# Kernel optimization log

Hardware: AMD Instinct MI355X
Metric: run time of the kernel (lower is better)

Reference implementation:

```python
import jax, jax.numpy as jnp
import numpy as np

N = 100000   # nodes
E = 1600000  # edges (avg degree 16)
D = 128      # input feature dim
H = 128      # Config.hidden_dim
G = 64       # graphs in batch
OUT = 2      # output classes


def setup_inputs() -> dict:
    key = jax.random.key(0)
    ks = jax.random.split(key, 12)
    s = 0.05
    return {
        "x": jax.random.normal(ks[0], (N, D), dtype=jnp.float32),
        "edge_index": jax.random.randint(ks[1], (2, E), 0, N),
        "batch": jnp.sort(jax.random.randint(ks[2], (N,), 0, G)),
        "W1": jax.random.normal(ks[3], (H, D), dtype=jnp.float32) * s,
        "b1": jnp.zeros((H,), jnp.float32),
        "W2": jax.random.normal(ks[4], (H, H), dtype=jnp.float32) * s,
        "b2": jnp.zeros((H,), jnp.float32),
        "Wf1": jax.random.normal(ks[5], (H, H), dtype=jnp.float32) * s,
        "bf1": jnp.zeros((H,), jnp.float32),
        "Wf2": jax.random.normal(ks[6], (OUT, H), dtype=jnp.float32) * s,
        "bf2": jnp.zeros((OUT,), jnp.float32),
    }


def _gnn_layer(x, src, dst, W, b):
    # message(x_j) = Linear(x[src]); linear commutes with gather, so transform
    # node features once (N rows) instead of per-edge (E rows): same math.
    xw = x @ W.T + b                                   # [N, H]
    msg = xw[src]                                      # [E, H] gather
    summed = jax.ops.segment_sum(msg, dst, num_segments=N)            # [N, H]
    cnt = jax.ops.segment_sum(jnp.ones((src.shape[0],), x.dtype), dst,
                              num_segments=N)                          # [N]
    return summed / jnp.maximum(cnt, 1.0)[:, None]     # scatter-mean (0 for deg-0)


def reference(x, edge_index, batch, W1, b1, W2, b2, Wf1, bf1, Wf2, bf2):
    src, dst = edge_index[0], edge_index[1]
    h = jax.nn.relu(_gnn_layer(x, src, dst, W1, b1))
    h = jax.nn.relu(_gnn_layer(h, src, dst, W2, b2))
    g = jax.ops.segment_max(h, batch, num_segments=G)  # global_max_pool [G, H]
    z = jax.nn.relu(g @ Wf1.T + bf1)                   # fc (dropout = identity, eval)
    z = z @ Wf2.T + bf2                                # [G, OUT]
    return jax.nn.log_softmax(z, axis=1)
```

## Files before the change

kernel.cpp:

```cpp
#include <hip/hip_runtime.h>
#include <hip/hip_fp16.h>
#include <math.h>


#define BUCKET_SHIFT 8
#define BUCKET_SIZE 256
#define MAXBUCK 512
#define BIN_CHUNK 4096
#define CAP 4608
#define LSTR 136

typedef _Float16 half8 __attribute__((ext_vector_type(8)));
typedef _Float16 half4v __attribute__((ext_vector_type(4)));
typedef _Float16 half2v __attribute__((ext_vector_type(2)));
typedef float floatx4 __attribute__((ext_vector_type(4)));
typedef float floatx2 __attribute__((ext_vector_type(2)));

#define RFL(v) __builtin_amdgcn_readfirstlane(v)

__global__ __launch_bounds__(256) void k_bin(
        const int* __restrict__ src, const int* __restrict__ dst,
        int* __restrict__ bcur, int* __restrict__ staging,
        const int* __restrict__ batch, int* __restrict__ gstart,
        int* __restrict__ gend,
        const float* __restrict__ W1, const float* __restrict__ W2,
        _Float16* __restrict__ w1h, _Float16* __restrict__ w2h,
        int E, int N, int nbuck) {
    __shared__ int lh[MAXBUCK];
    __shared__ int lbase[MAXBUCK];
    __shared__ int lc[MAXBUCK];
    int t = threadIdx.x;
    for (int i = t; i < nbuck; i += 256) { lh[i] = 0; lc[i] = 0; }

    if (blockIdx.x < 64) {
        int i = blockIdx.x * 256 + t;
        w1h[i] = (_Float16)W1[i];
        w2h[i] = (_Float16)W2[i];
    }

    int n = blockIdx.x * 256 + t;
    if (n < N) {
        int b = batch[n];
        if (n == 0 || batch[n - 1] != b) gstart[b] = n;
        if (n == N - 1 || batch[n + 1] != b) gend[b] = n + 1;
    }
    __syncthreads();

    int base = blockIdx.x * BIN_CHUNK;
    if (base + BIN_CHUNK <= E) {
        int ds[16], ss[16];
        const int4* dv = (const int4*)(dst + base);
        const int4* sv = (const int4*)(src + base);
        #pragma unroll
        for (int j = 0; j < 4; ++j) {
            int4 d = dv[j * 256 + t];
            int4 s = sv[j * 256 + t];
            ds[j * 4 + 0] = d.x; ds[j * 4 + 1] = d.y;
            ds[j * 4 + 2] = d.z; ds[j * 4 + 3] = d.w;
            ss[j * 4 + 0] = s.x; ss[j * 4 + 1] = s.y;
            ss[j * 4 + 2] = s.z; ss[j * 4 + 3] = s.w;
        }
        #pragma unroll
        for (int q = 0; q < 16; ++q)
            atomicAdd(&lh[ds[q] >> BUCKET_SHIFT], 1);
        __syncthreads();
        for (int i = t; i < nbuck; i += 256)
            if (lh[i]) lbase[i] = i * CAP + atomicAdd(&bcur[i], lh[i]);
        __syncthreads();
        #pragma unroll
        for (int q = 0; q < 16; ++q) {
            int d = ds[q];
            int b = d >> BUCKET_SHIFT;
            int pos = lbase[b] + atomicAdd(&lc[b], 1);
            if (pos < (b + 1) * CAP)
                staging[pos] = ss[q] | ((d & (BUCKET_SIZE - 1)) << 24);
        }
    } else {
        for (int e = base + t; e < E; e += 256)
            atomicAdd(&lh[dst[e] >> BUCKET_SHIFT], 1);
        __syncthreads();
        for (int i = t; i < nbuck; i += 256)
            if (lh[i]) lbase[i] = i * CAP + atomicAdd(&bcur[i], lh[i]);
        __syncthreads();
        for (int e = base + t; e < E; e += 256) {
            int d = dst[e];
            int b = d >> BUCKET_SHIFT;
            int pos = lbase[b] + atomicAdd(&lc[b], 1);
            if (pos < (b + 1) * CAP)
                staging[pos] = src[e] | ((d & (BUCKET_SIZE - 1)) << 24);
        }
    }
}

__global__ __launch_bounds__(BUCKET_SIZE) void k_bcsr(
        const int* __restrict__ staging, const int* __restrict__ bcur,
        int* __restrict__ esrc, int* __restrict__ rowstart,
        int* __restrict__ deg, int N) {
    __shared__ int sw[CAP];
    __shared__ int lh[BUCKET_SIZE];
    __shared__ int lcur[BUCKET_SIZE];
    __shared__ int wsum[4];
    int b = blockIdx.x;
    int s = b * CAP;
    int e = s + min(bcur[b], CAP);
    int len = e - s;
    int t = threadIdx.x;
    lh[t] = 0;
    __syncthreads();
    for (int i = t; i < len; i += BUCKET_SIZE) {
        int p = staging[s + i];
        sw[i] = p;
        atomicAdd(&lh[((unsigned)p) >> 24], 1);
    }
    __syncthreads();
    int v = lh[t];
    int lane = t & 63;
    int wv = t >> 6;
    int inc = v;
    #pragma unroll
    for (int off = 1; off < 64; off <<= 1) {
        int x = __shfl_up(inc, off, 64);
        if (lane >= off) inc += x;
    }
    if (lane == 63) wsum[wv] = inc;
    __syncthreads();
    int woff = 0;
    #pragma unroll
    for (int k = 0; k < 3; ++k)
        if (k < wv) woff += wsum[k];
    int excl = woff + inc - v;
    int node = b * BUCKET_SIZE + t;
    if (node < N) { rowstart[node] = s + excl; deg[node] = v; }
    lcur[t] = excl;
    __syncthreads();
    for (int i = t; i < len; i += BUCKET_SIZE) {
        int p = sw[i];
        int local = ((unsigned)p) >> 24;
        int pos = atomicAdd(&lcur[local], 1);
        esrc[s + pos] = p & 0xFFFFFF;
    }
}

template <typename T>
__global__ __launch_bounds__(512) void k_gemm(const T* __restrict__ in,
                                              const _Float16* __restrict__ Wh,
                                              const float* __restrict__ bias,
                                              unsigned char* __restrict__ out8,
                                              int N) {
    __shared__ _Float16 sX[128 * LSTR];
    __shared__ _Float16 sW[128 * LSTR];
    int t = threadIdx.x;

    #pragma unroll
    for (int it = 0; it < 8; ++it) {
        int lin = it * 512 + t;
        int r = lin >> 5;
        int c = (lin & 31) * 4;
        *(half4v*)&sW[r * LSTR + c] = *(const half4v*)(Wh + r * 128 + c);
    }

    int w = t >> 6;
    int lane = t & 63;
    int quad = lane >> 4;
    int lrow = lane & 15;

    #pragma unroll
    for (int tile = 0; tile < 2; ++tile) {
        int n0 = blockIdx.x * 256 + tile * 128;
        __syncthreads();
        #pragma unroll
        for (int it = 0; it < 8; ++it) {
            int lin = it * 512 + t;
            int r = lin >> 5;
            int c = (lin & 31) * 4;
            half4v xh = {0, 0, 0, 0};
            int n = n0 + r;
            if (n < N) {
                if constexpr (sizeof(T) == 4) {
                    float4 xv = *(const float4*)((const float*)in + (size_t)n * 128 + c);
                    xh = half4v{ (_Float16)xv.x, (_Float16)xv.y, (_Float16)xv.z, (_Float16)xv.w };
                } else {
                    xh = *(const half4v*)((const _Float16*)in + (size_t)n * 128 + c);
                }
            }
            *(half4v*)&sX[r * LSTR + c] = xh;
        }
        __syncthreads();

        floatx4 acc[8];
        #pragma unroll
        for (int i = 0; i < 8; ++i) acc[i] = {0.f, 0.f, 0.f, 0.f};

        int arow = (w * 16 + lrow) * LSTR + quad * 8;
        #pragma unroll
        for (int k0 = 0; k0 < 128; k0 += 32) {
            half8 a = *(const half8*)&sX[arow + k0];
            #pragma unroll
            for (int ht = 0; ht < 8; ++ht) {
                half8 bfr = *(const half8*)&sW[(ht * 16 + lrow) * LSTR + quad * 8 + k0];
                acc[ht] = __builtin_amdgcn_mfma_f32_16x16x32_f16(a, bfr, acc[ht], 0, 0, 0);
            }
        }

        #pragma unroll
        for (int ht = 0; ht < 8; ++ht) {
            int h = ht * 16 + lrow;
            float bv = bias[h];
            #pragma unroll
            for (int r = 0; r < 4; ++r) {
                int node = n0 + w * 16 + quad * 4 + r;
                if (node < N) {
                    float v = acc[ht][r] + bv;
                    int pk = __builtin_amdgcn_cvt_pk_fp8_f32(v, v, 0, false);
                    out8[(size_t)node * 128 + h] = (unsigned char)(pk & 0xFF);
                }
            }
        }
    }
}

__global__ __launch_bounds__(256) void k_agg(const unsigned char* __restrict__ in8,
                                             const int* __restrict__ esrc,
                                             const int* __restrict__ rowstart,
                                             const int* __restrict__ deg,
                                             _Float16* __restrict__ outh, int N) {
    int lane = threadIdx.x & 63;
    int node = blockIdx.x * 4 + (threadIdx.x >> 6);
    if (node >= N) return;
    int start = RFL(rowstart[node]);
    int d     = RFL(deg[node]);
    const unsigned short* in16 = (const unsigned short*)in8;

    floatx2 a0 = {0.f, 0.f}, a1 = {0.f, 0.f}, a2 = {0.f, 0.f}, a3 = {0.f, 0.f};

    int i = 0;
    for (; i + 8 <= d; i += 8) {
        int x0 = RFL(esrc[start + i + 0]);
        int x1 = RFL(esrc[start + i + 1]);
        int x2 = RFL(esrc[start + i + 2]);
        int x3 = RFL(esrc[start + i + 3]);
        int x4 = RFL(esrc[start + i + 4]);
        int x5 = RFL(esrc[start + i + 5]);
        int x6 = RFL(esrc[start + i + 6]);
        int x7 = RFL(esrc[start + i + 7]);
        unsigned u0 = in16[((size_t)x0 << 6) + lane];
        unsigned u1 = in16[((size_t)x1 << 6) + lane];
        unsigned u2 = in16[((size_t)x2 << 6) + lane];
        unsigned u3 = in16[((size_t)x3 << 6) + lane];
        unsigned u4 = in16[((size_t)x4 << 6) + lane];
        unsigned u5 = in16[((size_t)x5 << 6) + lane];
        unsigned u6 = in16[((size_t)x6 << 6) + lane];
        unsigned u7 = in16[((size_t)x7 << 6) + lane];
        floatx2 f0 = __builtin_amdgcn_cvt_pk_f32_fp8(u0, false);
        floatx2 f1 = __builtin_amdgcn_cvt_pk_f32_fp8(u1, false);
        floatx2 f2 = __builtin_amdgcn_cvt_pk_f32_fp8(u2, false);
        floatx2 f3 = __builtin_amdgcn_cvt_pk_f32_fp8(u3, false);
        floatx2 f4 = __builtin_amdgcn_cvt_pk_f32_fp8(u4, false);
        floatx2 f5 = __builtin_amdgcn_cvt_pk_f32_fp8(u5, false);
        floatx2 f6 = __builtin_amdgcn_cvt_pk_f32_fp8(u6, false);
        floatx2 f7 = __builtin_amdgcn_cvt_pk_f32_fp8(u7, false);
        a0.x += f0.x; a0.y += f0.y;  a1.x += f1.x; a1.y += f1.y;
        a2.x += f2.x; a2.y += f2.y;  a3.x += f3.x; a3.y += f3.y;
        a0.x += f4.x; a0.y += f4.y;  a1.x += f5.x; a1.y += f5.y;
        a2.x += f6.x; a2.y += f6.y;  a3.x += f7.x; a3.y += f7.y;
    }
    for (; i + 4 <= d; i += 4) {
        int x0 = RFL(esrc[start + i + 0]);
        int x1 = RFL(esrc[start + i + 1]);
        int x2 = RFL(esrc[start + i + 2]);
        int x3 = RFL(esrc[start + i + 3]);
        unsigned u0 = in16[((size_t)x0 << 6) + lane];
        unsigned u1 = in16[((size_t)x1 << 6) + lane];
        unsigned u2 = in16[((size_t)x2 << 6) + lane];
        unsigned u3 = in16[((size_t)x3 << 6) + lane];
        floatx2 f0 = __builtin_amdgcn_cvt_pk_f32_fp8(u0, false);
        floatx2 f1 = __builtin_amdgcn_cvt_pk_f32_fp8(u1, false);
        floatx2 f2 = __builtin_amdgcn_cvt_pk_f32_fp8(u2, false);
        floatx2 f3 = __builtin_amdgcn_cvt_pk_f32_fp8(u3, false);
        a0.x += f0.x; a0.y += f0.y;  a1.x += f1.x; a1.y += f1.y;
        a2.x += f2.x; a2.y += f2.y;  a3.x += f3.x; a3.y += f3.y;
    }
    for (; i < d; ++i) {
        int x0 = RFL(esrc[start + i]);
        unsigned u0 = in16[((size_t)x0 << 6) + lane];
        floatx2 f0 = __builtin_amdgcn_cvt_pk_f32_fp8(u0, false);
        a0.x += f0.x; a0.y += f0.y;
    }

    float sx = (a0.x + a1.x) + (a2.x + a3.x);
    float sy = (a0.y + a1.y) + (a2.y + a3.y);
    float dm = fmaxf((float)d, 1.0f);
    half2v r = { (_Float16)fmaxf(sx / dm, 0.f),
                 (_Float16)fmaxf(sy / dm, 0.f) };
    *(half2v*)(outh + (size_t)node * 128 + lane * 2) = r;
}

__global__ __launch_bounds__(256) void k_aggp2(const unsigned char* __restrict__ in8,
                                               const int* __restrict__ esrc,
                                               const int* __restrict__ rowstart,
                                               const int* __restrict__ deg,
                                               const int* __restrict__ batch,
                                               float* __restrict__ pm, int N) {
    int lane = threadIdx.x & 63;
    int gw = blockIdx.x * 4 + (threadIdx.x >> 6);
    int n0 = gw * 16;
    if (n0 >= N) return;
    int nend = min(n0 + 16, N);
    const unsigned short* in16 = (const unsigned short*)in8;

    int curg = RFL(batch[n0]);
    float mx = 0.f, my = 0.f;

    for (int node = n0; node < nend; ++node) {
        int g = RFL(batch[node]);
        if (g != curg) {
            int* pmi = (int*)(pm + (size_t)curg * 128 + lane * 2);
            atomicMax(pmi,     __float_as_int(mx));
            atomicMax(pmi + 1, __float_as_int(my));
            curg = g; mx = 0.f; my = 0.f;
        }
        int start = RFL(rowstart[node]);
        int d     = RFL(deg[node]);
        floatx2 a0 = {0.f, 0.f}, a1 = {0.f, 0.f}, a2 = {0.f, 0.f}, a3 = {0.f, 0.f};
        int i = 0;
        for (; i + 8 <= d; i += 8) {
            int x0 = RFL(esrc[start + i + 0]);
            int x1 = RFL(esrc[start + i + 1]);
            int x2 = RFL(esrc[start + i + 2]);
            int x3 = RFL(esrc[start + i + 3]);
            int x4 = RFL(esrc[start + i + 4]);
            int x5 = RFL(esrc[start + i + 5]);
            int x6 = RFL(esrc[start + i + 6]);
            int x7 = RFL(esrc[start + i + 7]);
            unsigned u0 = in16[((size_t)x0 << 6) + lane];
            unsigned u1 = in16[((size_t)x1 << 6) + lane];
            unsigned u2 = in16[((size_t)x2 << 6) + lane];
            unsigned u3 = in16[((size_t)x3 << 6) + lane];
            unsigned u4 = in16[((size_t)x4 << 6) + lane];
            unsigned u5 = in16[((size_t)x5 << 6) + lane];
            unsigned u6 = in16[((size_t)x6 << 6) + lane];
            unsigned u7 = in16[((size_t)x7 << 6) + lane];
            floatx2 f0 = __builtin_amdgcn_cvt_pk_f32_fp8(u0, false);
            floatx2 f1 = __builtin_amdgcn_cvt_pk_f32_fp8(u1, false);
            floatx2 f2 = __builtin_amdgcn_cvt_pk_f32_fp8(u2, false);
            floatx2 f3 = __builtin_amdgcn_cvt_pk_f32_fp8(u3, false);
            floatx2 f4 = __builtin_amdgcn_cvt_pk_f32_fp8(u4, false);
            floatx2 f5 = __builtin_amdgcn_cvt_pk_f32_fp8(u5, false);
            floatx2 f6 = __builtin_amdgcn_cvt_pk_f32_fp8(u6, false);
            floatx2 f7 = __builtin_amdgcn_cvt_pk_f32_fp8(u7, false);
            a0.x += f0.x; a0.y += f0.y;  a1.x += f1.x; a1.y += f1.y;
            a2.x += f2.x; a2.y += f2.y;  a3.x += f3.x; a3.y += f3.y;
            a0.x += f4.x; a0.y += f4.y;  a1.x += f5.x; a1.y += f5.y;
            a2.x += f6.x; a2.y += f6.y;  a3.x += f7.x; a3.y += f7.y;
        }
        for (; i + 4 <= d; i += 4) {
            int x0 = RFL(esrc[start + i + 0]);
            int x1 = RFL(esrc[start + i + 1]);
            int x2 = RFL(esrc[start + i + 2]);
            int x3 = RFL(esrc[start + i + 3]);
            unsigned u0 = in16[((size_t)x0 << 6) + lane];
            unsigned u1 = in16[((size_t)x1 << 6) + lane];
            unsigned u2 = in16[((size_t)x2 << 6) + lane];
            unsigned u3 = in16[((size_t)x3 << 6) + lane];
            floatx2 f0 = __builtin_amdgcn_cvt_pk_f32_fp8(u0, false);
            floatx2 f1 = __builtin_amdgcn_cvt_pk_f32_fp8(u1, false);
            floatx2 f2 = __builtin_amdgcn_cvt_pk_f32_fp8(u2, false);
            floatx2 f3 = __builtin_amdgcn_cvt_pk_f32_fp8(u3, false);
            a0.x += f0.x; a0.y += f0.y;  a1.x += f1.x; a1.y += f1.y;
            a2.x += f2.x; a2.y += f2.y;  a3.x += f3.x; a3.y += f3.y;
        }
        for (; i < d; ++i) {
            int x0 = RFL(esrc[start + i]);
            unsigned u0 = in16[((size_t)x0 << 6) + lane];
            floatx2 f0 = __builtin_amdgcn_cvt_pk_f32_fp8(u0, false);
            a0.x += f0.x; a0.y += f0.y;
        }
        float sx = (a0.x + a1.x) + (a2.x + a3.x);
        float sy = (a0.y + a1.y) + (a2.y + a3.y);
        float dm = fmaxf((float)d, 1.0f);
        mx = fmaxf(mx, fmaxf(sx / dm, 0.f));
        my = fmaxf(my, fmaxf(sy / dm, 0.f));
    }
    int* pmi = (int*)(pm + (size_t)curg * 128 + lane * 2);
    atomicMax(pmi,     __float_as_int(mx));
    atomicMax(pmi + 1, __float_as_int(my));
}

__global__ void k_fc(const float* __restrict__ pm,
                     const float* __restrict__ Wf1, const float* __restrict__ bf1,
                     const float* __restrict__ Wf2, const float* __restrict__ bf2,
                     float* __restrict__ out) {
    __shared__ float sg[128];
    __shared__ float sz[128];
    __shared__ float so[2];
    int g = blockIdx.x;
    int t = threadIdx.x;
    sg[t] = pm[(size_t)g * 128 + t];
    __syncthreads();
    float z = bf1[t];
    #pragma unroll 4
    for (int d = 0; d < 128; ++d)
        z += sg[d] * Wf1[t * 128 + d];
    sz[t] = fmaxf(z, 0.f);
    __syncthreads();
    if (t < 2) {
        float o = bf2[t];
        for (int d = 0; d < 128; ++d)
            o += sz[d] * Wf2[t * 128 + d];
        so[t] = o;
    }
    __syncthreads();
    if (t == 0) {
        float a = so[0], b = so[1];
        float mx = fmaxf(a, b);
        float ls = mx + logf(expf(a - mx) + expf(b - mx));
        out[g * 2 + 0] = a - ls;
        out[g * 2 + 1] = b - ls;
    }
}

extern "C" void kernel_launch(void* const* d_in, const int* in_sizes, int n_in,
                              void* d_out, int out_size, void* d_ws, size_t ws_size,
                              hipStream_t stream) {
    const float* x   = (const float*)d_in[0];
    const int*   ei  = (const int*)d_in[1];
    const int* batch = (const int*)d_in[2];
    const float* W1  = (const float*)d_in[3];
    const float* b1  = (const float*)d_in[4];
    const float* W2  = (const float*)d_in[5];
    const float* b2  = (const float*)d_in[6];
    const float* Wf1 = (const float*)d_in[7];
    const float* bf1 = (const float*)d_in[8];
    const float* Wf2 = (const float*)d_in[9];
    const float* bf2 = (const float*)d_in[10];

    int N = in_sizes[2];
    int E = in_sizes[1] / 2;
    int G = out_size / 2;
    const int* src = ei;
    const int* dst = ei + E;
    int nbuck = (N + BUCKET_SIZE - 1) / BUCKET_SIZE;

    char* p = (char*)d_ws;
    auto alloc = [&](size_t bytes) -> char* {
        char* r = p;
        p += (bytes + 255) & ~(size_t)255;
        return r;
    };
    unsigned char* A  = (unsigned char*)alloc((size_t)N * 128);
    unsigned char* A2 = (unsigned char*)alloc((size_t)N * 128);
    _Float16* B    = (_Float16*)alloc((size_t)N * 128 * 2);
    int* deg       = (int*)alloc((size_t)N * 4);
    int* rowstart  = (int*)alloc((size_t)N * 4);
    int* esrc      = (int*)alloc((size_t)nbuck * CAP * 4);
    int* staging   = (int*)alloc((size_t)nbuck * CAP * 4);
    _Float16* w1h  = (_Float16*)alloc((size_t)128 * 128 * 2);
    _Float16* w2h  = (_Float16*)alloc((size_t)128 * 128 * 2);
    char* zbase    = p;
    int* bcur      = (int*)alloc((size_t)MAXBUCK * 4);
    int* gstart    = (int*)alloc((size_t)G * 4);
    int* gend      = (int*)alloc((size_t)G * 4);
    float* pm      = (float*)alloc((size_t)G * 128 * 4);
    size_t zbytes  = (size_t)(p - zbase);

    int nchunk = (E + BIN_CHUNK - 1) / BIN_CHUNK;

    hipMemsetAsync(zbase, 0, zbytes, stream);
    k_bin<<<nchunk, 256, 0, stream>>>(src, dst, bcur, staging, batch,
                                      gstart, gend, W1, W2, w1h, w2h,
                                      E, N, nbuck);
    k_bcsr<<<nbuck, BUCKET_SIZE, 0, stream>>>(staging, bcur, esrc, rowstart, deg, N);

    k_gemm<float><<<(N + 255) / 256, 512, 0, stream>>>(x, w1h, b1, A, N);
    k_agg<<<(N + 3) / 4, 256, 0, stream>>>(A, esrc, rowstart, deg, B, N);
    k_gemm<_Float16><<<(N + 255) / 256, 512, 0, stream>>>(B, w2h, b2, A2, N);
    k_aggp2<<<(N + 63) / 64, 256, 0, stream>>>(A2, esrc, rowstart, deg, batch, pm, N);
    k_fc<<<G, 128, 0, stream>>>(pm, Wf1, bf1, Wf2, bf2, (float*)d_out);
}
```

Before: 284.0 us.

## Fuse layer-1 aggregation with layer-2 GEMM to skip fp16 intermediate

Merges the first scatter-mean aggregation kernel and the second-layer GEMM into one kernel. Each wave aggregates 16 nodes into shared memory, then runs MFMA against W2 read directly from global memory and writes fp8 output. This removes the N×128 fp16 intermediate buffer write and read and one kernel launch. In exchange each wave now processes 16 nodes serially before its GEMM step, so there are fewer waves in flight to hide gather latency, and W2 is no longer staged in LDS.

```diff
diff --git a/kernel.cpp b/kernel.cpp
--- a/kernel.cpp
+++ b/kernel.cpp
@@ -141,8 +141,7 @@
     }
 }
 
-template <typename T>
-__global__ __launch_bounds__(512) void k_gemm(const T* __restrict__ in,
+__global__ __launch_bounds__(512) void k_gemm(const float* __restrict__ in,
                                               const _Float16* __restrict__ Wh,
                                               const float* __restrict__ bias,
                                               unsigned char* __restrict__ out8,
@@ -176,12 +175,8 @@
             half4v xh = {0, 0, 0, 0};
             int n = n0 + r;
             if (n < N) {
-                if constexpr (sizeof(T) == 4) {
-                    float4 xv = *(const float4*)((const float*)in + (size_t)n * 128 + c);
-                    xh = half4v{ (_Float16)xv.x, (_Float16)xv.y, (_Float16)xv.z, (_Float16)xv.w };
-                } else {
-                    xh = *(const half4v*)((const _Float16*)in + (size_t)n * 128 + c);
-                }
+                float4 xv = *(const float4*)(in + (size_t)n * 128 + c);
+                xh = half4v{ (_Float16)xv.x, (_Float16)xv.y, (_Float16)xv.z, (_Float16)xv.w };
             }
             *(half4v*)&sX[r * LSTR + c] = xh;
         }
@@ -219,80 +214,123 @@
     }
 }
 
-__global__ __launch_bounds__(256) void k_agg(const unsigned char* __restrict__ in8,
+__global__ __launch_bounds__(256) void k_agf(const unsigned char* __restrict__ in8,
                                              const int* __restrict__ esrc,
                                              const int* __restrict__ rowstart,
                                              const int* __restrict__ deg,
-                                             _Float16* __restrict__ outh, int N) {
-    int lane = threadIdx.x & 63;
-    int node = blockIdx.x * 4 + (threadIdx.x >> 6);
-    if (node >= N) return;
-    int start = RFL(rowstart[node]);
-    int d     = RFL(deg[node]);
+                                             const _Float16* __restrict__ w2h,
+                                             const float* __restrict__ b2,
+                                             unsigned char* __restrict__ out8,
+                                             int N) {
+    __shared__ _Float16 sX[64 * LSTR];
+    int t = threadIdx.x;
+    int w = t >> 6;
+    int lane = t & 63;
+    int n0 = blockIdx.x * 64 + w * 16;
     const unsigned short* in16 = (const unsigned short*)in8;
 
-    floatx2 a0 = {0.f, 0.f}, a1 = {0.f, 0.f}, a2 = {0.f, 0.f}, a3 = {0.f, 0.f};
-
-    int i = 0;
-    for (; i + 8 <= d; i += 8) {
-        int x0 = RFL(esrc[start + i + 0]);
-        int x1 = RFL(esrc[start + i + 1]);
-        int x2 = RFL(esrc[start + i + 2]);
-        int x3 = RFL(esrc[start + i + 3]);
-        int x4 = RFL(esrc[start + i + 4]);
-        int x5 = RFL(esrc[start + i + 5]);
-        int x6 = RFL(esrc[start + i + 6]);
-        int x7 = RFL(esrc[start + i + 7]);
-        unsigned u0 = in16[((size_t)x0 << 6) + lane];
-        unsigned u1 = in16[((size_t)x1 << 6) + lane];
-        unsigned u2 = in16[((size_t)x2 << 6) + lane];
-        unsigned u3 = in16[((size_t)x3 << 6) + lane];
-        unsigned u4 = in16[((size_t)x4 << 6) + lane];
-        unsigned u5 = in16[((size_t)x5 << 6) + lane];
-        unsigned u6 = in16[((size_t)x6 << 6) + lane];
-        unsigned u7 = in16[((size_t)x7 << 6) + lane];
-        floatx2 f0 = __builtin_amdgcn_cvt_pk_f32_fp8(u0, false);
-        floatx2 f1 = __builtin_amdgcn_cvt_pk_f32_fp8(u1, false);
-        floatx2 f2 = __builtin_amdgcn_cvt_pk_f32_fp8(u2, false);
-        floatx2 f3 = __builtin_amdgcn_cvt_pk_f32_fp8(u3, false);
-        floatx2 f4 = __builtin_amdgcn_cvt_pk_f32_fp8(u4, false);
-        floatx2 f5 = __builtin_amdgcn_cvt_pk_f32_fp8(u5, false);
-        floatx2 f6 = __builtin_amdgcn_cvt_pk_f32_fp8(u6, false);
-        floatx2 f7 = __builtin_amdgcn_cvt_pk_f32_fp8(u7, false);
-        a0.x += f0.x; a0.y += f0.y;  a1.x += f1.x; a1.y += f1.y;
-        a2.x += f2.x; a2.y += f2.y;  a3.x += f3.x; a3.y += f3.y;
-        a0.x += f4.x; a0.y += f4.y;  a1.x += f5.x; a1.y += f5.y;
-        a2.x += f6.x; a2.y += f6.y;  a3.x += f7.x; a3.y += f7.y;
-    }
-    for (; i + 4 <= d; i += 4) {
-        int x0 = RFL(esrc[start + i + 0]);
-        int x1 = RFL(esrc[start + i + 1]);
-        int x2 = RFL(esrc[start + i + 2]);
-        int x3 = RFL(esrc[start + i + 3]);
-        unsigned u0 = in16[((size_t)x0 << 6) + lane];
-        unsigned u1 = in16[((size_t)x1 << 6) + lane];
-        unsigned u2 = in16[((size_t)x2 << 6) + lane];
-        unsigned u3 = in16[((size_t)x3 << 6) + lane];
-        floatx2 f0 = __builtin_amdgcn_cvt_pk_f32_fp8(u0, false);
-        floatx2 f1 = __builtin_amdgcn_cvt_pk_f32_fp8(u1, false);
-        floatx2 f2 = __builtin_amdgcn_cvt_pk_f32_fp8(u2, false);
-        floatx2 f3 = __builtin_amdgcn_cvt_pk_f32_fp8(u3, false);
-        a0.x += f0.x; a0.y += f0.y;  a1.x += f1.x; a1.y += f1.y;
-        a2.x += f2.x; a2.y += f2.y;  a3.x += f3.x; a3.y += f3.y;
-    }
-    for (; i < d; ++i) {
-        int x0 = RFL(esrc[start + i]);
-        unsigned u0 = in16[((size_t)x0 << 6) + lane];
-        floatx2 f0 = __builtin_amdgcn_cvt_pk_f32_fp8(u0, false);
-        a0.x += f0.x; a0.y += f0.y;
-    }
-
-    float sx = (a0.x + a1.x) + (a2.x + a3.x);
-    float sy = (a0.y + a1.y) + (a2.y + a3.y);
-    float dm = fmaxf((float)d, 1.0f);
-    half2v r = { (_Float16)fmaxf(sx / dm, 0.f),
-                 (_Float16)fmaxf(sy / dm, 0.f) };
-    *(half2v*)(outh + (size_t)node * 128 + lane * 2) = r;
+    for (int k = 0; k < 16; ++k) {
+        int node = n0 + k;
+        float sx = 0.f, sy = 0.f;
+        int dd = 0;
+        if (node < N) {
+            int start = RFL(rowstart[node]);
+            int d     = RFL(deg[node]);
+            dd = d;
+            floatx2 a0 = {0.f, 0.f}, a1 = {0.f, 0.f}, a2 = {0.f, 0.f}, a3 = {0.f, 0.f};
+            int i = 0;
+            for (; i + 8 <= d; i += 8) {
+                int x0 = RFL(esrc[start + i + 0]);
+                int x1 = RFL(esrc[start + i + 1]);
+                int x2 = RFL(esrc[start + i + 2]);
+                int x3 = RFL(esrc[start + i + 3]);
+                int x4 = RFL(esrc[start + i + 4]);
+                int x5 = RFL(esrc[start + i + 5]);
+                int x6 = RFL(esrc[start + i + 6]);
+                int x7 = RFL(esrc[start + i + 7]);
+                unsigned u0 = in16[((size_t)x0 << 6) + lane];
+                unsigned u1 = in16[((size_t)x1 << 6) + lane];
+                unsigned u2 = in16[((size_t)x2 << 6) + lane];
+                unsigned u3 = in16[((size_t)x3 << 6) + lane];
+                unsigned u4 = in16[((size_t)x4 << 6) + lane];
+                unsigned u5 = in16[((size_t)x5 << 6) + lane];
+                unsigned u6 = in16[((size_t)x6 << 6) + lane];
+                unsigned u7 = in16[((size_t)x7 << 6) + lane];
+                floatx2 f0 = __builtin_amdgcn_cvt_pk_f32_fp8(u0, false);
+                floatx2 f1 = __builtin_amdgcn_cvt_pk_f32_fp8(u1, false);
+                floatx2 f2 = __builtin_amdgcn_cvt_pk_f32_fp8(u2, false);
+                floatx2 f3 = __builtin_amdgcn_cvt_pk_f32_fp8(u3, false);
+                floatx2 f4 = __builtin_amdgcn_cvt_pk_f32_fp8(u4, false);
+                floatx2 f5 = __builtin_amdgcn_cvt_pk_f32_fp8(u5, false);
+                floatx2 f6 = __builtin_amdgcn_cvt_pk_f32_fp8(u6, false);
+                floatx2 f7 = __builtin_amdgcn_cvt_pk_f32_fp8(u7, false);
+                a0.x += f0.x; a0.y += f0.y;  a1.x += f1.x; a1.y += f1.y;
+                a2.x += f2.x; a2.y += f2.y;  a3.x += f3.x; a3.y += f3.y;
+                a0.x += f4.x; a0.y += f4.y;  a1.x += f5.x; a1.y += f5.y;
+                a2.x += f6.x; a2.y += f6.y;  a3.x += f7.x; a3.y += f7.y;
+            }
+            for (; i + 4 <= d; i += 4) {
+                int x0 = RFL(esrc[start + i + 0]);
+                int x1 = RFL(esrc[start + i + 1]);
+                int x2 = RFL(esrc[start + i + 2]);
+                int x3 = RFL(esrc[start + i + 3]);
+                unsigned u0 = in16[((size_t)x0 << 6) + lane];
+                unsigned u1 = in16[((size_t)x1 << 6) + lane];
+                unsigned u2 = in16[((size_t)x2 << 6) + lane];
+                unsigned u3 = in16[((size_t)x3 << 6) + lane];
+                floatx2 f0 = __builtin_amdgcn_cvt_pk_f32_fp8(u0, false);
+                floatx2 f1 = __builtin_amdgcn_cvt_pk_f32_fp8(u1, false);
+                floatx2 f2 = __builtin_amdgcn_cvt_pk_f32_fp8(u2, false);
+                floatx2 f3 = __builtin_amdgcn_cvt_pk_f32_fp8(u3, false);
+                a0.x += f0.x; a0.y += f0.y;  a1.x += f1.x; a1.y += f1.y;
+                a2.x += f2.x; a2.y += f2.y;  a3.x += f3.x; a3.y += f3.y;
+            }
+            for (; i < d; ++i) {
+                int x0 = RFL(esrc[start + i]);
+                unsigned u0 = in16[((size_t)x0 << 6) + lane];
+                floatx2 f0 = __builtin_amdgcn_cvt_pk_f32_fp8(u0, false);
+                a0.x += f0.x; a0.y += f0.y;
+            }
+            sx = (a0.x + a1.x) + (a2.x + a3.x);
+            sy = (a0.y + a1.y) + (a2.y + a3.y);
+        }
+        float dm = fmaxf((float)dd, 1.0f);
+        half2v hv = { (_Float16)fmaxf(sx / dm, 0.f),
+                      (_Float16)fmaxf(sy / dm, 0.f) };
+        *(half2v*)&sX[(w * 16 + k) * LSTR + lane * 2] = hv;
+    }
+    __syncthreads();
+
+    int quad = lane >> 4;
+    int lrow = lane & 15;
+    floatx4 acc[8];
+    #pragma unroll
+    for (int i = 0; i < 8; ++i) acc[i] = {0.f, 0.f, 0.f, 0.f};
+
+    int arow = (w * 16 + lrow) * LSTR + quad * 8;
+    #pragma unroll
+    for (int k0 = 0; k0 < 128; k0 += 32) {
+        half8 a = *(const half8*)&sX[arow + k0];
+        #pragma unroll
+        for (int ht = 0; ht < 8; ++ht) {
+            half8 b = *(const half8*)(w2h + (ht * 16 + lrow) * 128 + quad * 8 + k0);
+            acc[ht] = __builtin_amdgcn_mfma_f32_16x16x32_f16(a, b, acc[ht], 0, 0, 0);
+        }
+    }
+    #pragma unroll
+    for (int ht = 0; ht < 8; ++ht) {
+        int h = ht * 16 + lrow;
+        float bv = b2[h];
+        #pragma unroll
+        for (int r = 0; r < 4; ++r) {
+            int node = n0 + quad * 4 + r;
+            if (node < N) {
+                float v = acc[ht][r] + bv;
+                int pk = __builtin_amdgcn_cvt_pk_fp8_f32(v, v, 0, false);
+                out8[(size_t)node * 128 + h] = (unsigned char)(pk & 0xFF);
+            }
+        }
+    }
 }
 
 __global__ __launch_bounds__(256) void k_aggp2(const unsigned char* __restrict__ in8,
@@ -449,7 +487,6 @@
     };
     unsigned char* A  = (unsigned char*)alloc((size_t)N * 128);
     unsigned char* A2 = (unsigned char*)alloc((size_t)N * 128);
-    _Float16* B    = (_Float16*)alloc((size_t)N * 128 * 2);
     int* deg       = (int*)alloc((size_t)N * 4);
     int* rowstart  = (int*)alloc((size_t)N * 4);
     int* esrc      = (int*)alloc((size_t)nbuck * CAP * 4);
@@ -471,9 +508,8 @@
                                       E, N, nbuck);
     k_bcsr<<<nbuck, BUCKET_SIZE, 0, stream>>>(staging, bcur, esrc, rowstart, deg, N);
 
-    k_gemm<float><<<(N + 255) / 256, 512, 0, stream>>>(x, w1h, b1, A, N);
-    k_agg<<<(N + 3) / 4, 256, 0, stream>>>(A, esrc, rowstart, deg, B, N);
-    k_gemm<_Float16><<<(N + 255) / 256, 512, 0, stream>>>(B, w2h, b2, A2, N);
+    k_gemm<<<(N + 255) / 256, 512, 0, stream>>>(x, w1h, b1, A, N);
+    k_agf<<<(N + 63) / 64, 256, 0, stream>>>(A, esrc, rowstart, deg, w2h, b2, A2, N);
     k_aggp2<<<(N + 63) / 64, 256, 0, stream>>>(A2, esrc, rowstart, deg, batch, pm, N);
     k_fc<<<G, 128, 0, stream>>>(pm, Wf1, bf1, Wf2, bf2, (float*)d_out);
 }
```

Result: slower. 324.0 us (+14.1%).
